# Optimization experiments

Hardware: AMD Instinct MI355X
Metric: run time of the kernel (lower is better)

The kernel has to match this reference:

```python
import jax, jax.numpy as jnp
import numpy as np

F = 26
D = 128
B = 16384
# upper-triangular (offset=1) index pairs over (F+1)x(F+1)
_TRIU_I, _TRIU_J = np.triu_indices(F + 1, k=1)
_TRIU_I = jnp.asarray(_TRIU_I)
_TRIU_J = jnp.asarray(_TRIU_J)


def setup_inputs() -> dict:
    key = jax.random.key(0)
    k1, k2 = jax.random.split(key)
    sparse_x = jax.random.normal(k1, (B, F, D), dtype=jnp.float32)
    dense_x = jax.random.normal(k2, (B, D), dtype=jnp.float32)
    return {"sparse_x": sparse_x, "dense_x": dense_x}


def reference(sparse_x, dense_x):
    # combined: [B, F+1, D] -- dense feature appended as one extra row
    combined = jnp.concatenate([sparse_x, dense_x[:, None, :]], axis=1)
    # pairwise dot products: [B, F+1, F+1]
    interact = jnp.einsum('bfd,bgd->bfg', combined, combined)
    # gather strict upper triangle -> [B, K] where K = (F+1)*F/2
    return interact[:, _TRIU_I, _TRIU_J]
```

## Files before the change

### kernel.cpp

```cpp
#include <hip/hip_runtime.h>

constexpr int kRows   = 27;
constexpr int kD      = 128;
constexpr int kKP     = 136;
constexpr int kSlot   = 32 * kKP;
constexpr int kNB     = 4;
constexpr int kPairs  = 351;

typedef __attribute__((ext_vector_type(8))) short bf16x8;
typedef __attribute__((ext_vector_type(4))) float f32x4;

__device__ __forceinline__ unsigned short to_bf16(float f) {
    union { float f; unsigned u; } x; x.f = f;
    unsigned u = x.u;
    return (unsigned short)((u + 0x7fffu + ((u >> 16) & 1u)) >> 16);
}

__device__ __forceinline__ int triu_idx(int i, int j) {
    return (i * (53 - i)) / 2 + (j - i - 1);
}

__global__ __launch_bounds__(256) void interact_kernel(
    const float* __restrict__ sparse_x,
    const float* __restrict__ dense_x,
    float* __restrict__ out)
{
    __shared__ short lds[kNB * kSlot];
    const int t  = threadIdx.x;
    const int b0 = blockIdx.x * kNB;

    {
        const ushort4 z = {0, 0, 0, 0};
        #pragma unroll
        for (int e = t; e < 640; e += 256) {
            const int slot = e / 160;
            const int rem  = e - slot * 160;
            const int row  = 27 + (rem >> 5);
            const int c4   = (rem & 31) * 4;
            *reinterpret_cast<ushort4*>(&lds[slot * kSlot + row * kKP + c4]) = z;
        }
    }

    const float4* sp = reinterpret_cast<const float4*>(sparse_x + (size_t)b0 * (26 * kD));
    #pragma unroll
    for (int it = 0; it < 13; ++it) {
        const int e = t + it * 256;
        float4 v = sp[e];
        const int f    = e * 4;
        const int slot = f / 3328;
        const int rem  = f - slot * 3328;
        const int row  = rem >> 7;
        const int col  = rem & 127;
        ushort4 h;
        h.x = to_bf16(v.x); h.y = to_bf16(v.y);
        h.z = to_bf16(v.z); h.w = to_bf16(v.w);
        *reinterpret_cast<ushort4*>(&lds[slot * kSlot + row * kKP + col]) = h;
    }
    if (t < 32 * kNB) {
        const int slot = t >> 5;
        const int c4   = (t & 31) * 4;
        float4 v = *reinterpret_cast<const float4*>(dense_x + (size_t)(b0 + slot) * kD + c4);
        ushort4 h;
        h.x = to_bf16(v.x); h.y = to_bf16(v.y);
        h.z = to_bf16(v.z); h.w = to_bf16(v.w);
        *reinterpret_cast<ushort4*>(&lds[slot * kSlot + 26 * kKP + c4]) = h;
    }
    __syncthreads();

    const int wave = t >> 6;
    const int lane = t & 63;
    const short* X = &lds[wave * kSlot];
    const int m    = lane & 15;
    const int quad = lane >> 4;

    f32x4 c00 = {0.f, 0.f, 0.f, 0.f};
    f32x4 c01 = {0.f, 0.f, 0.f, 0.f};
    f32x4 c11 = {0.f, 0.f, 0.f, 0.f};

    #pragma unroll
    for (int k0 = 0; k0 < kD; k0 += 32) {
        bf16x8 a0 = *reinterpret_cast<const bf16x8*>(&X[m * kKP + quad * 8 + k0]);
        bf16x8 a1 = *reinterpret_cast<const bf16x8*>(&X[(16 + m) * kKP + quad * 8 + k0]);
        c00 = __builtin_amdgcn_mfma_f32_16x16x32_bf16(a0, a0, c00, 0, 0, 0);
        c01 = __builtin_amdgcn_mfma_f32_16x16x32_bf16(a0, a1, c01, 0, 0, 0);
        c11 = __builtin_amdgcn_mfma_f32_16x16x32_bf16(a1, a1, c11, 0, 0, 0);
    }

    float* ob = out + (size_t)(b0 + wave) * kPairs;
    const int j = m;
    #pragma unroll
    for (int r = 0; r < 4; ++r) {
        const int i = quad * 4 + r;
        if (i < j)                        ob[triu_idx(i, j)]           = c00[r];
        if (16 + j < kRows)               ob[triu_idx(i, 16 + j)]      = c01[r];
        if (i < j && 16 + j < kRows)      ob[triu_idx(16 + i, 16 + j)] = c11[r];
    }
}

extern "C" void kernel_launch(void* const* d_in, const int* in_sizes, int n_in,
                              void* d_out, int out_size, void* d_ws, size_t ws_size,
                              hipStream_t stream) {
    const float* sparse_x = (const float*)d_in[0];
    const float* dense_x  = (const float*)d_in[1];
    float* out = (float*)d_out;
    const int B = in_sizes[1] / kD;
    interact_kernel<<<B / kNB, 256, 0, stream>>>(sparse_x, dense_x, out);
}
```

Measured before the change: 305.3 us.

## Load MFMA operands directly from global into registers and stage output via LDS

Removes the LDS staging of bf16-converted inputs. Each lane now loads its fp32 row fragments straight from global memory into registers and packs them to bf16 for the MFMA, which drops the cross-wave __syncthreads and the zero-padding pass. The scattered triangular output writes now go to a per-wave LDS buffer first and are then copied to global contiguously, giving coalesced stores. A launch_bounds occupancy hint is added as well. The per-lane global loads are 32-byte strided fragments that may coalesce less well than the old linear loads, and register pressure goes up.

```diff
diff --git a/kernel.cpp b/kernel.cpp
--- a/kernel.cpp
+++ b/kernel.cpp
@@ -1,100 +1,93 @@
 #include <hip/hip_runtime.h>
+#include <hip/hip_bf16.h>
 
-constexpr int kRows   = 27;
-constexpr int kD      = 128;
-constexpr int kKP     = 136;
-constexpr int kSlot   = 32 * kKP;
-constexpr int kNB     = 4;
-constexpr int kPairs  = 351;
+constexpr int kRows  = 27;
+constexpr int kD     = 128;
+constexpr int kPairs = 351;
+constexpr int kNB    = 4;
 
 typedef __attribute__((ext_vector_type(8))) short bf16x8;
 typedef __attribute__((ext_vector_type(4))) float f32x4;
 
-__device__ __forceinline__ unsigned short to_bf16(float f) {
-    union { float f; unsigned u; } x; x.f = f;
-    unsigned u = x.u;
-    return (unsigned short)((u + 0x7fffu + ((u >> 16) & 1u)) >> 16);
+__device__ __forceinline__ short bfs(float x) {
+    union { __hip_bfloat16 h; short s; } u;
+    u.h = __float2bfloat16(x);
+    return u.s;
+}
+
+__device__ __forceinline__ bf16x8 pack8(float4 a, float4 b) {
+    bf16x8 r;
+    r[0] = bfs(a.x); r[1] = bfs(a.y); r[2] = bfs(a.z); r[3] = bfs(a.w);
+    r[4] = bfs(b.x); r[5] = bfs(b.y); r[6] = bfs(b.z); r[7] = bfs(b.w);
+    return r;
 }
 
 __device__ __forceinline__ int triu_idx(int i, int j) {
     return (i * (53 - i)) / 2 + (j - i - 1);
 }
 
-__global__ __launch_bounds__(256) void interact_kernel(
+__global__ __launch_bounds__(256, 4) void interact_kernel(
     const float* __restrict__ sparse_x,
     const float* __restrict__ dense_x,
     float* __restrict__ out)
 {
-    __shared__ short lds[kNB * kSlot];
-    const int t  = threadIdx.x;
-    const int b0 = blockIdx.x * kNB;
-
-    {
-        const ushort4 z = {0, 0, 0, 0};
-        #pragma unroll
-        for (int e = t; e < 640; e += 256) {
-            const int slot = e / 160;
-            const int rem  = e - slot * 160;
-            const int row  = 27 + (rem >> 5);
-            const int c4   = (rem & 31) * 4;
-            *reinterpret_cast<ushort4*>(&lds[slot * kSlot + row * kKP + c4]) = z;
-        }
-    }
-
-    const float4* sp = reinterpret_cast<const float4*>(sparse_x + (size_t)b0 * (26 * kD));
-    #pragma unroll
-    for (int it = 0; it < 13; ++it) {
-        const int e = t + it * 256;
-        float4 v = sp[e];
-        const int f    = e * 4;
-        const int slot = f / 3328;
-        const int rem  = f - slot * 3328;
-        const int row  = rem >> 7;
-        const int col  = rem & 127;
-        ushort4 h;
-        h.x = to_bf16(v.x); h.y = to_bf16(v.y);
-        h.z = to_bf16(v.z); h.w = to_bf16(v.w);
-        *reinterpret_cast<ushort4*>(&lds[slot * kSlot + row * kKP + col]) = h;
-    }
-    if (t < 32 * kNB) {
-        const int slot = t >> 5;
-        const int c4   = (t & 31) * 4;
-        float4 v = *reinterpret_cast<const float4*>(dense_x + (size_t)(b0 + slot) * kD + c4);
-        ushort4 h;
-        h.x = to_bf16(v.x); h.y = to_bf16(v.y);
-        h.z = to_bf16(v.z); h.w = to_bf16(v.w);
-        *reinterpret_cast<ushort4*>(&lds[slot * kSlot + 26 * kKP + c4]) = h;
-    }
-    __syncthreads();
-
+    __shared__ float obuf[kNB][kPairs + 1];
+    const int t    = threadIdx.x;
     const int wave = t >> 6;
     const int lane = t & 63;
-    const short* X = &lds[wave * kSlot];
     const int m    = lane & 15;
     const int quad = lane >> 4;
+    const int batch = blockIdx.x * kNB + wave;
+
+    const float* sb = sparse_x + (size_t)batch * (26 * kD);
+    const int c0 = quad * 8;
+
+    float4 f0[8];
+    const float* p0 = sb + m * kD + c0;
+    #pragma unroll
+    for (int k = 0; k < 4; ++k) {
+        f0[2 * k]     = *reinterpret_cast<const float4*>(p0 + k * 32);
+        f0[2 * k + 1] = *reinterpret_cast<const float4*>(p0 + k * 32 + 4);
+    }
+    float4 f1[8];
+    const int r = 16 + m;
+    if (r < kRows) {
+        const float* p1 = (r < 26 ? sb + r * kD
+                                  : dense_x + (size_t)batch * kD) + c0;
+        #pragma unroll
+        for (int k = 0; k < 4; ++k) {
+            f1[2 * k]     = *reinterpret_cast<const float4*>(p1 + k * 32);
+            f1[2 * k + 1] = *reinterpret_cast<const float4*>(p1 + k * 32 + 4);
+        }
+    } else {
+        const float4 z = {0.f, 0.f, 0.f, 0.f};
+        #pragma unroll
+        for (int k = 0; k < 8; ++k) f1[k] = z;
+    }
 
     f32x4 c00 = {0.f, 0.f, 0.f, 0.f};
     f32x4 c01 = {0.f, 0.f, 0.f, 0.f};
     f32x4 c11 = {0.f, 0.f, 0.f, 0.f};
-
     #pragma unroll
-    for (int k0 = 0; k0 < kD; k0 += 32) {
-        bf16x8 a0 = *reinterpret_cast<const bf16x8*>(&X[m * kKP + quad * 8 + k0]);
-        bf16x8 a1 = *reinterpret_cast<const bf16x8*>(&X[(16 + m) * kKP + quad * 8 + k0]);
+    for (int k = 0; k < 4; ++k) {
+        bf16x8 a0 = pack8(f0[2 * k], f0[2 * k + 1]);
+        bf16x8 a1 = pack8(f1[2 * k], f1[2 * k + 1]);
         c00 = __builtin_amdgcn_mfma_f32_16x16x32_bf16(a0, a0, c00, 0, 0, 0);
         c01 = __builtin_amdgcn_mfma_f32_16x16x32_bf16(a0, a1, c01, 0, 0, 0);
         c11 = __builtin_amdgcn_mfma_f32_16x16x32_bf16(a1, a1, c11, 0, 0, 0);
     }
 
-    float* ob = out + (size_t)(b0 + wave) * kPairs;
+    float* ob = obuf[wave];
     const int j = m;
     #pragma unroll
-    for (int r = 0; r < 4; ++r) {
-        const int i = quad * 4 + r;
-        if (i < j)                        ob[triu_idx(i, j)]           = c00[r];
-        if (16 + j < kRows)               ob[triu_idx(i, 16 + j)]      = c01[r];
-        if (i < j && 16 + j < kRows)      ob[triu_idx(16 + i, 16 + j)] = c11[r];
+    for (int rr = 0; rr < 4; ++rr) {
+        const int i = quad * 4 + rr;
+        if (i < j)                        ob[triu_idx(i, j)]           = c00[rr];
+        if (16 + j < kRows)               ob[triu_idx(i, 16 + j)]      = c01[rr];
+        if (i < j && 16 + j < kRows)      ob[triu_idx(16 + i, 16 + j)] = c11[rr];
     }
+    float* og = out + (size_t)batch * kPairs;
+    for (int e = lane; e < kPairs; e += 64) og[e] = ob[e];
 }
 
 extern "C" void kernel_launch(void* const* d_in, const int* in_sizes, int n_in,
```

Result: no change. 307.6 us (+0.7%).
